# Optimization experiments

Hardware: AMD Instinct MI355X
Metric: run time of the kernel (lower is better)

Reference implementation:

```python
import jax, jax.numpy as jnp
import numpy as np

NEG_SLOPE = 0.2  # both GATConv internal LeakyReLU and the module-level activation


def gat_conv(x, src, dst, W, a_src, a_dst, bias):
    """PyG GATConv (concat=True, add_self_loops handled by caller via src/dst).
    x: [N, Din]; W: [Din, H*C]; a_src, a_dst: [H, C]; bias: [H*C]."""
    N = x.shape[0]
    H, C = a_src.shape
    h = (x @ W).reshape(N, H, C)                       # [N, H, C]
    al_src = jnp.einsum('nhc,hc->nh', h, a_src)        # [N, H]
    al_dst = jnp.einsum('nhc,hc->nh', h, a_dst)        # [N, H]
    e = jax.nn.leaky_relu(al_src[src] + al_dst[dst], NEG_SLOPE)  # [E, H]
    # segment softmax over edges grouped by destination node
    m = jax.ops.segment_max(e, dst, num_segments=N)    # [N, H]
    ex = jnp.exp(e - m[dst])
    denom = jax.ops.segment_sum(ex, dst, num_segments=N)
    alpha = ex / denom[dst]                            # [E, H]
    out = jax.ops.segment_sum(alpha[:, :, None] * h[src], dst, num_segments=N)
    return out.reshape(N, H * C) + bias


def setup_inputs() -> dict:
    key = jax.random.key(0)
    N, E = 50000, 800000
    D_IN, HID, H = 128, 128, 2
    C = HID // H
    ks = jax.random.split(key, 20)
    inp = {
        'x': jax.random.normal(ks[0], (N, D_IN), dtype=jnp.float32),
        'edge_index': jax.random.randint(ks[1], (2, E), 0, N, dtype=jnp.int64),
    }
    dims = [D_IN, HID, HID]  # input dims of the 3 GATConv layers
    for i, din in enumerate(dims, start=1):
        s = 1.0 / np.sqrt(din)
        inp[f'W{i}'] = jax.random.normal(ks[2 + 4 * i], (din, HID), dtype=jnp.float32) * s
        inp[f'a_src{i}'] = jax.random.normal(ks[3 + 4 * i], (H, C), dtype=jnp.float32) * 0.1
        inp[f'a_dst{i}'] = jax.random.normal(ks[4 + 4 * i], (H, C), dtype=jnp.float32) * 0.1
        inp[f'b{i}'] = jnp.zeros((HID,), dtype=jnp.float32)
    inp['lin_w'] = jax.random.normal(ks[2], (HID, 1), dtype=jnp.float32) * (1.0 / np.sqrt(HID))
    inp['lin_b'] = jnp.zeros((1,), dtype=jnp.float32)
    return inp


def reference(x, edge_index, W1, a_src1, a_dst1, b1, W2, a_src2, a_dst2, b2,
              W3, a_src3, a_dst3, b3, lin_w, lin_b):
    N = x.shape[0]
    loops = jnp.arange(N, dtype=edge_index.dtype)
    src = jnp.concatenate([edge_index[0], loops])  # add_self_loops=True
    dst = jnp.concatenate([edge_index[1], loops])

    h = jax.nn.leaky_relu(gat_conv(x, src, dst, W1, a_src1, a_dst1, b1), NEG_SLOPE)
    # dropout is identity in eval mode (p=0.0)
    h = jax.nn.leaky_relu(h + gat_conv(h, src, dst, W2, a_src2, a_dst2, b2), NEG_SLOPE)
    h = jax.nn.leaky_relu(h + gat_conv(h, src, dst, W3, a_src3, a_dst3, b3), NEG_SLOPE)
    logits = (h @ lin_w + lin_b).squeeze(-1)  # [N]
    return logits
```

## Files before the change

### kernel.cpp

```cpp
#include <hip/hip_runtime.h>
#include <hip/hip_bf16.h>
#include <hip/hip_fp16.h>

#define LEAK 0.2f

typedef _Float16 half8  __attribute__((ext_vector_type(8)));
typedef _Float16 half4v __attribute__((ext_vector_type(4)));
typedef float    float4v __attribute__((ext_vector_type(4)));


__global__ __launch_bounds__(256) void k_bincount(const int* __restrict__ edst,
                                                  int* __restrict__ gbkt,
                                                  int E, int ETOT, int NBK) {
    __shared__ int lh[512];
    int t = threadIdx.x;
    for (int b = t; b < NBK; b += 256) lh[b] = 0;
    __syncthreads();
    int base = blockIdx.x * 4096;
    #pragma unroll
    for (int u = 0; u < 16; ++u) {
        int e = base + u * 256 + t;
        if (e < ETOT) {
            int d = (e < E) ? edst[e] : (e - E);
            atomicAdd(&lh[d >> 7], 1);
        }
    }
    __syncthreads();
    for (int b = t; b < NBK; b += 256)
        if (lh[b]) atomicAdd(&gbkt[b], lh[b]);
}

__global__ __launch_bounds__(512) void k_bktscan(const int* __restrict__ gbkt,
                                                 int* __restrict__ bko,
                                                 int* __restrict__ gcur, int NBK) {
    int t = threadIdx.x;
    int v = (t < NBK) ? gbkt[t] : 0;
    int lane = t & 63, wid = t >> 6;
    int x = v;
    #pragma unroll
    for (int o = 1; o < 64; o <<= 1) {
        int y = __shfl_up(x, o);
        if (lane >= o) x += y;
    }
    __shared__ int ws[8];
    if (lane == 63) ws[wid] = x;
    __syncthreads();
    if (wid == 0) {
        int s = (lane < 8) ? ws[lane] : 0;
        #pragma unroll
        for (int o = 1; o < 8; o <<= 1) {
            int y = __shfl_up(s, o);
            if (lane >= o) s += y;
        }
        if (lane < 8) ws[lane] = s;
    }
    __syncthreads();
    int excl = x - v + (wid > 0 ? ws[wid - 1] : 0);
    if (t < NBK) { bko[t] = excl; gcur[t] = excl; }
    if (t == 511) bko[NBK] = excl;
}

__global__ __launch_bounds__(256) void k_binscatter(const int* __restrict__ esrc,
                                                    const int* __restrict__ edst,
                                                    int* __restrict__ gcur,
                                                    unsigned int* __restrict__ binned,
                                                    int E, int ETOT, int NBK) {
    __shared__ int lh[512];
    __shared__ int lbase[512];
    int t = threadIdx.x;
    for (int b = t; b < NBK; b += 256) lh[b] = 0;
    __syncthreads();
    int base = blockIdx.x * 4096;
    unsigned int word[16]; int bb[16], rk[16];
    #pragma unroll
    for (int u = 0; u < 16; ++u) {
        int e = base + u * 256 + t;
        bb[u] = -1;
        if (e < ETOT) {
            int s, d;
            if (e < E) { s = esrc[e]; d = edst[e]; } else { s = d = e - E; }
            int b = d >> 7;
            bb[u] = b;
            rk[u] = atomicAdd(&lh[b], 1);
            word[u] = (unsigned int)s | ((unsigned int)(d & 127) << 17);
        }
    }
    __syncthreads();
    for (int b = t; b < NBK; b += 256) {
        int c = lh[b];
        lbase[b] = c ? atomicAdd(&gcur[b], c) : 0;
    }
    __syncthreads();
    #pragma unroll
    for (int u = 0; u < 16; ++u)
        if (bb[u] >= 0) binned[lbase[bb[u]] + rk[u]] = word[u];
}

__global__ __launch_bounds__(256) void k_scatter2(const unsigned int* __restrict__ binned,
                                                  const int* __restrict__ bko,
                                                  int* __restrict__ off,
                                                  int* __restrict__ csr, int N, int NBK) {
    __shared__ int deg[128];
    __shared__ int lcur[128];
    __shared__ int wt[2];
    int b = blockIdx.x, t = threadIdx.x;
    int n0 = b << 7;
    if (t < 128) deg[t] = 0;
    __syncthreads();
    int beg = bko[b], end = bko[b + 1];
    for (int i = beg + t; i < end; i += 256)
        atomicAdd(&deg[binned[i] >> 17], 1);
    __syncthreads();
    int v = 0, x = 0;
    if (t < 128) {
        v = deg[t];
        x = v;
        int lane = t & 63;
        #pragma unroll
        for (int o = 1; o < 64; o <<= 1) {
            int y = __shfl_up(x, o);
            if (lane >= o) x += y;
        }
        if (lane == 63) wt[t >> 6] = x;
    }
    __syncthreads();
    if (t < 128) {
        int excl = x - v + ((t >= 64) ? wt[0] : 0) + beg;
        lcur[t] = excl;
        int node = n0 + t;
        if (node < N) off[node] = excl;
    }
    if (b == NBK - 1 && t == 0) off[N] = end;
    __syncthreads();
    for (int i = beg + t; i < end; i += 256) {
        unsigned int u = binned[i];
        int pos = atomicAdd(&lcur[u >> 17], 1);
        csr[pos] = (int)(u & 0x1FFFF);
    }
}


__global__ __launch_bounds__(256) void k_wconv(const float* __restrict__ W0,
                                               const float* __restrict__ W1,
                                               const float* __restrict__ W2,
                                               _Float16* __restrict__ w16t) {
    __shared__ _Float16 tile[64][68];
    int m = blockIdx.x >> 2;
    int ti = (blockIdx.x >> 1) & 1, tj = blockIdx.x & 1;
    const float* src = (m == 0) ? W0 : (m == 1 ? W1 : W2);
    _Float16* dst = w16t + m * 16384;
    int t = threadIdx.x;
    for (int idx = t; idx < 4096; idx += 256) {
        int r = idx >> 6, c = idx & 63;
        tile[r][c] = (_Float16)src[(ti * 64 + r) * 128 + tj * 64 + c];
    }
    __syncthreads();
    for (int idx = t; idx < 4096; idx += 256) {
        int c = idx >> 6, r = idx & 63;
        dst[(tj * 64 + c) * 128 + ti * 64 + r] = tile[r][c];
    }
}


__global__ __launch_bounds__(256) void k_gemm_mfma(const void* __restrict__ Xv, int xfp16,
                                                   const _Float16* __restrict__ WhT,
                                                   const float* __restrict__ a_src,
                                                   const float* __restrict__ a_dst,
                                                   _Float16* __restrict__ Hout,
                                                   float* __restrict__ alsrc,
                                                   float* __restrict__ aldst, int N) {
    __shared__ _Float16 As[64][136];
    __shared__ float sS[64][2];
    __shared__ float sD[64][2];
    const int t = threadIdx.x;
    const int lane = t & 63, w = t >> 6;
    const int block_row = blockIdx.x * 64;

    if (t < 128) { sS[t >> 1][t & 1] = 0.f; sD[t >> 1][t & 1] = 0.f; }

    if (xfp16) {
        const _Float16* Xh = (const _Float16*)Xv;
        #pragma unroll
        for (int it = 0; it < 4; ++it) {
            int i = t + 256 * it;
            int row = i >> 4, c8 = i & 15;
            int gr = block_row + row;
            half8 hv = (half8){0,0,0,0,0,0,0,0};
            if (gr < N) hv = *(const half8*)(Xh + (size_t)gr * 128 + c8 * 8);
            *(half8*)(&As[row][c8 * 8]) = hv;
        }
    } else {
        const float* X = (const float*)Xv;
        #pragma unroll
        for (int it = 0; it < 8; ++it) {
            int i = t + 256 * it;
            int row = i >> 5, c4 = i & 31;
            int gr = block_row + row;
            float4 xv = make_float4(0.f, 0.f, 0.f, 0.f);
            if (gr < N) xv = *(const float4*)(X + (size_t)gr * 128 + c4 * 4);
            half4v hv;
            hv[0] = (_Float16)xv.x; hv[1] = (_Float16)xv.y;
            hv[2] = (_Float16)xv.z; hv[3] = (_Float16)xv.w;
            *(half4v*)(&As[row][c4 * 4]) = hv;
        }
    }

    const int l15 = lane & 15, kq = (lane >> 4) * 8;
    half8 bf[2][4];
    #pragma unroll
    for (int ntl = 0; ntl < 2; ++ntl) {
        int n0 = (w * 2 + ntl) * 16 + l15;
        #pragma unroll
        for (int kt = 0; kt < 4; ++kt)
            bf[ntl][kt] = *(const half8*)(WhT + (size_t)n0 * 128 + kt * 32 + kq);
    }
    __syncthreads();

    float4v acc[4][2];
    #pragma unroll
    for (int mt = 0; mt < 4; ++mt)
        #pragma unroll
        for (int ntl = 0; ntl < 2; ++ntl)
            acc[mt][ntl] = (float4v){0.f, 0.f, 0.f, 0.f};

    #pragma unroll
    for (int kt = 0; kt < 4; ++kt) {
        half8 a[4];
        #pragma unroll
        for (int mt = 0; mt < 4; ++mt)
            a[mt] = *(const half8*)(&As[mt * 16 + l15][kt * 32 + kq]);
        #pragma unroll
        for (int mt = 0; mt < 4; ++mt)
            #pragma unroll
            for (int ntl = 0; ntl < 2; ++ntl)
                acc[mt][ntl] = __builtin_amdgcn_mfma_f32_16x16x32_f16(
                    a[mt], bf[ntl][kt], acc[mt][ntl], 0, 0, 0);
    }

    #pragma unroll
    for (int mt = 0; mt < 4; ++mt) {
        int r0 = block_row + mt * 16 + (lane >> 4) * 4;
        #pragma unroll
        for (int ntl = 0; ntl < 2; ++ntl) {
            int col = (w * 2 + ntl) * 16 + l15;
            #pragma unroll
            for (int reg = 0; reg < 4; ++reg) {
                int r = r0 + reg;
                if (r < N) Hout[(size_t)r * 128 + col] = (_Float16)acc[mt][ntl][reg];
            }
        }
    }

    {
        int c0 = w * 32 + l15, c1 = c0 + 16;
        float as0 = a_src[c0], as1 = a_src[c1];
        float ad0 = a_dst[c0], ad1 = a_dst[c1];
        int head = w >> 1;
        #pragma unroll
        for (int mt = 0; mt < 4; ++mt) {
            #pragma unroll
            for (int reg = 0; reg < 4; ++reg) {
                float ps = (float)acc[mt][0][reg] * as0 + (float)acc[mt][1][reg] * as1;
                float pd = (float)acc[mt][0][reg] * ad0 + (float)acc[mt][1][reg] * ad1;
                #pragma unroll
                for (int o = 1; o < 16; o <<= 1) {
                    ps += __shfl_xor(ps, o);
                    pd += __shfl_xor(pd, o);
                }
                if (l15 == 0) {
                    int row = mt * 16 + (lane >> 4) * 4 + reg;
                    atomicAdd(&sS[row][head], ps);
                    atomicAdd(&sD[row][head], pd);
                }
            }
        }
    }
    __syncthreads();
    if (t < 128) {
        int row = t >> 1, head = t & 1;
        int gr = block_row + row;
        if (gr < N) {
            alsrc[gr * 2 + head] = sS[row][head];
            aldst[gr * 2 + head] = sD[row][head];
        }
    }
}


__global__ __launch_bounds__(256) void k_aggregate(
        const _Float16* __restrict__ H16,
        const float* __restrict__ alsrc,
        const float* __restrict__ aldst,
        const int* __restrict__ off, const int* __restrict__ csr,
        const float* __restrict__ bias,
        const _Float16* __restrict__ prev,
        _Float16* __restrict__ Out,
        const float* __restrict__ lw, const float* __restrict__ lb,
        float* __restrict__ logits, int N, int mode) {
    int wglobal = (int)((blockIdx.x * 256 + threadIdx.x) >> 6);
    int lane = threadIdx.x & 63;
    if (wglobal * 2 >= N) return;
    int half = lane >> 5;
    int hl = lane & 31;
    int node = wglobal * 2 + half;
    bool active = node < N;
    int nodeC = active ? node : (N - 1);
    int beg = off[nodeC];
    int end = active ? off[nodeC + 1] : beg;
    float ad0 = aldst[nodeC * 2], ad1 = aldst[nodeC * 2 + 1];

    int p = hl & 15;
    int q = hl >> 4;
    bool head0 = p < 8;
    const _Float16* hbase = H16 + p * 8;
    int hb = half << 5;

    float acc[8];
    #pragma unroll
    for (int k = 0; k < 8; ++k) acc[k] = 0.f;
    float dsum = 0.f;

    for (int base = beg; base < end; base += 32) {
        int i = base + hl;
        int s = 0; float w0 = 0.f, w1 = 0.f;
        if (i < end) {
            s = csr[i];
            float2 al = *(const float2*)(&alsrc[s * 2]);
            float e0 = al.x + ad0; e0 = e0 > 0.f ? e0 : LEAK * e0;
            float e1 = al.y + ad1; e1 = e1 > 0.f ? e1 : LEAK * e1;
            w0 = __expf(e0); w1 = __expf(e1);
        }
        int cnt = min(32, end - base);
        int iters = (cnt + 1) >> 1;
        int jj = 0;
        for (; jj + 4 <= iters; jj += 4) {
            int sl0 = hb + (jj << 1) + q;
            int sj0 = __shfl(s, sl0), sj1 = __shfl(s, sl0 + 2);
            int sj2 = __shfl(s, sl0 + 4), sj3 = __shfl(s, sl0 + 6);
            float w00 = __shfl(w0, sl0),     w10 = __shfl(w1, sl0);
            float w01 = __shfl(w0, sl0 + 2), w11 = __shfl(w1, sl0 + 2);
            float w02 = __shfl(w0, sl0 + 4), w12 = __shfl(w1, sl0 + 4);
            float w03 = __shfl(w0, sl0 + 6), w13 = __shfl(w1, sl0 + 6);
            float ws0 = head0 ? w00 : w10;
            float ws1 = head0 ? w01 : w11;
            float ws2 = head0 ? w02 : w12;
            float ws3 = head0 ? w03 : w13;
            uint4 r0 = *(const uint4*)(hbase + (size_t)sj0 * 128);
            uint4 r1 = *(const uint4*)(hbase + (size_t)sj1 * 128);
            uint4 r2 = *(const uint4*)(hbase + (size_t)sj2 * 128);
            uint4 r3 = *(const uint4*)(hbase + (size_t)sj3 * 128);
            const _Float16* h0 = (const _Float16*)&r0;
            const _Float16* h1 = (const _Float16*)&r1;
            const _Float16* h2 = (const _Float16*)&r2;
            const _Float16* h3 = (const _Float16*)&r3;
            #pragma unroll
            for (int k = 0; k < 8; ++k) acc[k] += ws0 * (float)h0[k];
            #pragma unroll
            for (int k = 0; k < 8; ++k) acc[k] += ws1 * (float)h1[k];
            #pragma unroll
            for (int k = 0; k < 8; ++k) acc[k] += ws2 * (float)h2[k];
            #pragma unroll
            for (int k = 0; k < 8; ++k) acc[k] += ws3 * (float)h3[k];
            dsum += (ws0 + ws1) + (ws2 + ws3);
        }
        for (; jj + 2 <= iters; jj += 2) {
            int sl0 = hb + (jj << 1) + q;
            int sj0 = __shfl(s, sl0), sj1 = __shfl(s, sl0 + 2);
            float w00 = __shfl(w0, sl0),     w10 = __shfl(w1, sl0);
            float w01 = __shfl(w0, sl0 + 2), w11 = __shfl(w1, sl0 + 2);
            float ws0 = head0 ? w00 : w10;
            float ws1 = head0 ? w01 : w11;
            uint4 r0 = *(const uint4*)(hbase + (size_t)sj0 * 128);
            uint4 r1 = *(const uint4*)(hbase + (size_t)sj1 * 128);
            const _Float16* h0 = (const _Float16*)&r0;
            const _Float16* h1 = (const _Float16*)&r1;
            #pragma unroll
            for (int k = 0; k < 8; ++k) acc[k] += ws0 * (float)h0[k];
            #pragma unroll
            for (int k = 0; k < 8; ++k) acc[k] += ws1 * (float)h1[k];
            dsum += ws0 + ws1;
        }
        if (jj < iters) {
            int sl = hb + (jj << 1) + q;
            int   sj = __shfl(s,  sl);
            float wa = __shfl(w0, sl);
            float wb = __shfl(w1, sl);
            float ws = head0 ? wa : wb;
            uint4 raw = *(const uint4*)(hbase + (size_t)sj * 128);
            const _Float16* h = (const _Float16*)&raw;
            #pragma unroll
            for (int k = 0; k < 8; ++k) acc[k] += ws * (float)h[k];
            dsum += ws;
        }
    }

    #pragma unroll
    for (int k = 0; k < 8; ++k) acc[k] += __shfl_xor(acc[k], 16);
    dsum += __shfl_xor(dsum, 16);

    if (q == 0 && active) {
        float inv = 1.f / dsum;
        int c0 = p * 8;
        float v[8];
        #pragma unroll
        for (int k = 0; k < 8; ++k) v[k] = acc[k] * inv + bias[c0 + k];
        if (mode >= 1) {
            half8 pv = *(const half8*)(prev + (size_t)node * 128 + c0);
            #pragma unroll
            for (int k = 0; k < 8; ++k) v[k] += (float)pv[k];
        }
        #pragma unroll
        for (int k = 0; k < 8; ++k) v[k] = v[k] > 0.f ? v[k] : LEAK * v[k];
        if (mode == 2) {
            float partial = 0.f;
            #pragma unroll
            for (int k = 0; k < 8; ++k) partial += v[k] * lw[c0 + k];
            partial += __shfl_xor(partial, 1);
            partial += __shfl_xor(partial, 2);
            partial += __shfl_xor(partial, 4);
            partial += __shfl_xor(partial, 8);
            if (hl == 0) logits[node] = partial + lb[0];
        } else {
            half8 ov;
            #pragma unroll
            for (int k = 0; k < 8; ++k) ov[k] = (_Float16)v[k];
            *(half8*)(Out + (size_t)node * 128 + c0) = ov;
        }
    }
}


extern "C" void kernel_launch(void* const* d_in, const int* in_sizes, int n_in,
                              void* d_out, int out_size, void* d_ws, size_t ws_size,
                              hipStream_t stream) {
    const float* x    = (const float*)d_in[0];
    const int*   edge = (const int*)d_in[1];
    const float* W[3]  = {(const float*)d_in[2], (const float*)d_in[6], (const float*)d_in[10]};
    const float* as[3] = {(const float*)d_in[3], (const float*)d_in[7], (const float*)d_in[11]};
    const float* ad[3] = {(const float*)d_in[4], (const float*)d_in[8], (const float*)d_in[12]};
    const float* bs[3] = {(const float*)d_in[5], (const float*)d_in[9], (const float*)d_in[13]};
    const float* lw = (const float*)d_in[14];
    const float* lb = (const float*)d_in[15];

    const int N    = in_sizes[0] / 128;
    const int E    = in_sizes[1] / 2;
    const int ETOT = E + N;
    const int NBK  = (N + 127) >> 7;

    char* base = (char*)d_ws;
    size_t o = 0;
    auto carve = [&](size_t bytes) {
        char* p = base + o;
        o = (o + bytes + 255) & ~(size_t)255;
        return p;
    };
    int*      off    = (int*)     carve((size_t)(N + 1) * 4);
    int*      gbkt   = (int*)     carve((size_t)(NBK + 1) * 4);
    int*      bko    = (int*)     carve((size_t)(NBK + 1) * 4);
    int*      gcur   = (int*)     carve((size_t)(NBK + 1) * 4);
    unsigned* binned = (unsigned*)carve((size_t)ETOT * 4);
    int*      csr    = (int*)     carve((size_t)ETOT * 4);
    float*    alsrc  = (float*)   carve((size_t)N * 2 * 4);
    float*    aldst  = (float*)   carve((size_t)N * 2 * 4);
    _Float16* h16    = (_Float16*)carve((size_t)N * 128 * 2);
    _Float16* bufA   = (_Float16*)carve((size_t)N * 128 * 2);
    _Float16* bufB   = (_Float16*)carve((size_t)N * 128 * 2);
    _Float16* w16t   = (_Float16*)carve((size_t)3 * 16384 * 2);
    (void)ws_size; (void)n_in; (void)out_size;

    const int* esrc = edge;
    const int* edst = edge + E;

    int eb = (ETOT + 4095) / 4096;

    hipMemsetAsync(gbkt, 0, (size_t)(NBK + 1) * 4, stream);
    k_wconv<<<12, 256, 0, stream>>>(W[0], W[1], W[2], w16t);

    k_bincount<<<eb, 256, 0, stream>>>(edst, gbkt, E, ETOT, NBK);
    k_bktscan<<<1, 512, 0, stream>>>(gbkt, bko, gcur, NBK);
    k_binscatter<<<eb, 256, 0, stream>>>(esrc, edst, gcur, binned, E, ETOT, NBK);
    k_scatter2<<<NBK, 256, 0, stream>>>(binned, bko, off, csr, N, NBK);

    int gemm_blocks = (N + 63) / 64;
    int agg_blocks  = (N + 7) / 8;

    k_gemm_mfma<<<gemm_blocks, 256, 0, stream>>>(x, 0, w16t, as[0], ad[0], h16, alsrc, aldst, N);
    k_aggregate<<<agg_blocks, 256, 0, stream>>>(h16, alsrc, aldst, off, csr,
                                                bs[0], nullptr, bufA, lw, lb, nullptr, N, 0);
    k_gemm_mfma<<<gemm_blocks, 256, 0, stream>>>(bufA, 1, w16t + 16384, as[1], ad[1], h16, alsrc, aldst, N);
    k_aggregate<<<agg_blocks, 256, 0, stream>>>(h16, alsrc, aldst, off, csr,
                                                bs[1], bufA, bufB, lw, lb, nullptr, N, 1);
    k_gemm_mfma<<<gemm_blocks, 256, 0, stream>>>(bufB, 1, w16t + 32768, as[2], ad[2], h16, alsrc, aldst, N);
    k_aggregate<<<agg_blocks, 256, 0, stream>>>(h16, alsrc, aldst, off, csr,
                                                bs[2], bufB, nullptr, lw, lb, (float*)d_out, N, 2);
}
```

Baseline: 291.1 us.

## Use fixed-capacity destination buckets to drop bincount and scan kernels

Replaces the two-pass bucket count plus prefix scan with fixed-capacity per-bucket regions (BCAP slots each), so binscatter writes directly at bucket*BCAP and scatter2 reads per-bucket counts. CSR now stores separate begin and end arrays per node since segments are no longer contiguous. The weight fp16 transpose is folded into extra blocks of the binscatter launch, removing another launch. It risks overflow if any bucket of 128 destination nodes receives more than BCAP edges, and it uses more workspace memory.

```diff
diff --git a/kernel.cpp b/kernel.cpp
--- a/kernel.cpp
+++ b/kernel.cpp
@@ -3,71 +3,43 @@
 #include <hip/hip_fp16.h>
 
 #define LEAK 0.2f
+#define BCAP 4096
 
 typedef _Float16 half8  __attribute__((ext_vector_type(8)));
 typedef _Float16 half4v __attribute__((ext_vector_type(4)));
 typedef float    float4v __attribute__((ext_vector_type(4)));
 
 
-__global__ __launch_bounds__(256) void k_bincount(const int* __restrict__ edst,
-                                                  int* __restrict__ gbkt,
-                                                  int E, int ETOT, int NBK) {
-    __shared__ int lh[512];
-    int t = threadIdx.x;
-    for (int b = t; b < NBK; b += 256) lh[b] = 0;
-    __syncthreads();
-    int base = blockIdx.x * 4096;
-    #pragma unroll
-    for (int u = 0; u < 16; ++u) {
-        int e = base + u * 256 + t;
-        if (e < ETOT) {
-            int d = (e < E) ? edst[e] : (e - E);
-            atomicAdd(&lh[d >> 7], 1);
-        }
-    }
-    __syncthreads();
-    for (int b = t; b < NBK; b += 256)
-        if (lh[b]) atomicAdd(&gbkt[b], lh[b]);
-}
-
-__global__ __launch_bounds__(512) void k_bktscan(const int* __restrict__ gbkt,
-                                                 int* __restrict__ bko,
-                                                 int* __restrict__ gcur, int NBK) {
-    int t = threadIdx.x;
-    int v = (t < NBK) ? gbkt[t] : 0;
-    int lane = t & 63, wid = t >> 6;
-    int x = v;
-    #pragma unroll
-    for (int o = 1; o < 64; o <<= 1) {
-        int y = __shfl_up(x, o);
-        if (lane >= o) x += y;
-    }
-    __shared__ int ws[8];
-    if (lane == 63) ws[wid] = x;
-    __syncthreads();
-    if (wid == 0) {
-        int s = (lane < 8) ? ws[lane] : 0;
-        #pragma unroll
-        for (int o = 1; o < 8; o <<= 1) {
-            int y = __shfl_up(s, o);
-            if (lane >= o) s += y;
-        }
-        if (lane < 8) ws[lane] = s;
-    }
-    __syncthreads();
-    int excl = x - v + (wid > 0 ? ws[wid - 1] : 0);
-    if (t < NBK) { bko[t] = excl; gcur[t] = excl; }
-    if (t == 511) bko[NBK] = excl;
-}
-
 __global__ __launch_bounds__(256) void k_binscatter(const int* __restrict__ esrc,
                                                     const int* __restrict__ edst,
-                                                    int* __restrict__ gcur,
+                                                    int* __restrict__ gcnt,
                                                     unsigned int* __restrict__ binned,
-                                                    int E, int ETOT, int NBK) {
+                                                    int E, int ETOT, int NBK, int eb,
+                                                    const float* __restrict__ W0,
+                                                    const float* __restrict__ W1,
+                                                    const float* __restrict__ W2,
+                                                    _Float16* __restrict__ w16t) {
+    int t = threadIdx.x;
+    if (blockIdx.x >= eb) {
+        __shared__ _Float16 tile[64][68];
+        int bb = blockIdx.x - eb;
+        int m = bb >> 2;
+        int ti = (bb >> 1) & 1, tj = bb & 1;
+        const float* src = (m == 0) ? W0 : (m == 1 ? W1 : W2);
+        _Float16* dst = w16t + m * 16384;
+        for (int idx = t; idx < 4096; idx += 256) {
+            int r = idx >> 6, c = idx & 63;
+            tile[r][c] = (_Float16)src[(ti * 64 + r) * 128 + tj * 64 + c];
+        }
+        __syncthreads();
+        for (int idx = t; idx < 4096; idx += 256) {
+            int c = idx >> 6, r = idx & 63;
+            dst[(tj * 64 + c) * 128 + ti * 64 + r] = tile[r][c];
+        }
+        return;
+    }
     __shared__ int lh[512];
     __shared__ int lbase[512];
-    int t = threadIdx.x;
     for (int b = t; b < NBK; b += 256) lh[b] = 0;
     __syncthreads();
     int base = blockIdx.x * 4096;
@@ -88,18 +60,20 @@
     __syncthreads();
     for (int b = t; b < NBK; b += 256) {
         int c = lh[b];
-        lbase[b] = c ? atomicAdd(&gcur[b], c) : 0;
+        lbase[b] = c ? atomicAdd(&gcnt[b], c) : 0;
     }
     __syncthreads();
     #pragma unroll
     for (int u = 0; u < 16; ++u)
-        if (bb[u] >= 0) binned[lbase[bb[u]] + rk[u]] = word[u];
+        if (bb[u] >= 0)
+            binned[(size_t)bb[u] * BCAP + lbase[bb[u]] + rk[u]] = word[u];
 }
 
 __global__ __launch_bounds__(256) void k_scatter2(const unsigned int* __restrict__ binned,
-                                                  const int* __restrict__ bko,
+                                                  const int* __restrict__ gcnt,
                                                   int* __restrict__ off,
-                                                  int* __restrict__ csr, int N, int NBK) {
+                                                  int* __restrict__ endv,
+                                                  int* __restrict__ csr, int N) {
     __shared__ int deg[128];
     __shared__ int lcur[128];
     __shared__ int wt[2];
@@ -107,7 +81,7 @@
     int n0 = b << 7;
     if (t < 128) deg[t] = 0;
     __syncthreads();
-    int beg = bko[b], end = bko[b + 1];
+    int beg = b * BCAP, end = beg + gcnt[b];
     for (int i = beg + t; i < end; i += 256)
         atomicAdd(&deg[binned[i] >> 17], 1);
     __syncthreads();
@@ -128,36 +102,13 @@
         int excl = x - v + ((t >= 64) ? wt[0] : 0) + beg;
         lcur[t] = excl;
         int node = n0 + t;
-        if (node < N) off[node] = excl;
-    }
-    if (b == NBK - 1 && t == 0) off[N] = end;
+        if (node < N) { off[node] = excl; endv[node] = excl + v; }
+    }
     __syncthreads();
     for (int i = beg + t; i < end; i += 256) {
         unsigned int u = binned[i];
         int pos = atomicAdd(&lcur[u >> 17], 1);
         csr[pos] = (int)(u & 0x1FFFF);
-    }
-}
-
-
-__global__ __launch_bounds__(256) void k_wconv(const float* __restrict__ W0,
-                                               const float* __restrict__ W1,
-                                               const float* __restrict__ W2,
-                                               _Float16* __restrict__ w16t) {
-    __shared__ _Float16 tile[64][68];
-    int m = blockIdx.x >> 2;
-    int ti = (blockIdx.x >> 1) & 1, tj = blockIdx.x & 1;
-    const float* src = (m == 0) ? W0 : (m == 1 ? W1 : W2);
-    _Float16* dst = w16t + m * 16384;
-    int t = threadIdx.x;
-    for (int idx = t; idx < 4096; idx += 256) {
-        int r = idx >> 6, c = idx & 63;
-        tile[r][c] = (_Float16)src[(ti * 64 + r) * 128 + tj * 64 + c];
-    }
-    __syncthreads();
-    for (int idx = t; idx < 4096; idx += 256) {
-        int c = idx >> 6, r = idx & 63;
-        dst[(tj * 64 + c) * 128 + ti * 64 + r] = tile[r][c];
     }
 }
 
@@ -291,7 +242,8 @@
         const _Float16* __restrict__ H16,
         const float* __restrict__ alsrc,
         const float* __restrict__ aldst,
-        const int* __restrict__ off, const int* __restrict__ csr,
+        const int* __restrict__ off, const int* __restrict__ endv,
+        const int* __restrict__ csr,
         const float* __restrict__ bias,
         const _Float16* __restrict__ prev,
         _Float16* __restrict__ Out,
@@ -306,7 +258,7 @@
     bool active = node < N;
     int nodeC = active ? node : (N - 1);
     int beg = off[nodeC];
-    int end = active ? off[nodeC + 1] : beg;
+    int end = active ? endv[nodeC] : beg;
     float ad0 = aldst[nodeC * 2], ad1 = aldst[nodeC * 2 + 1];
 
     int p = hl & 15;
@@ -454,12 +406,11 @@
         o = (o + bytes + 255) & ~(size_t)255;
         return p;
     };
-    int*      off    = (int*)     carve((size_t)(N + 1) * 4);
-    int*      gbkt   = (int*)     carve((size_t)(NBK + 1) * 4);
-    int*      bko    = (int*)     carve((size_t)(NBK + 1) * 4);
-    int*      gcur   = (int*)     carve((size_t)(NBK + 1) * 4);
-    unsigned* binned = (unsigned*)carve((size_t)ETOT * 4);
-    int*      csr    = (int*)     carve((size_t)ETOT * 4);
+    int*      off    = (int*)     carve((size_t)N * 4);
+    int*      endv   = (int*)     carve((size_t)N * 4);
+    int*      gcnt   = (int*)     carve((size_t)NBK * 4);
+    unsigned* binned = (unsigned*)carve((size_t)NBK * BCAP * 4);
+    int*      csr    = (int*)     carve((size_t)NBK * BCAP * 4);
     float*    alsrc  = (float*)   carve((size_t)N * 2 * 4);
     float*    aldst  = (float*)   carve((size_t)N * 2 * 4);
     _Float16* h16    = (_Float16*)carve((size_t)N * 128 * 2);
@@ -473,24 +424,22 @@
 
     int eb = (ETOT + 4095) / 4096;
 
-    hipMemsetAsync(gbkt, 0, (size_t)(NBK + 1) * 4, stream);
-    k_wconv<<<12, 256, 0, stream>>>(W[0], W[1], W[2], w16t);
-
-    k_bincount<<<eb, 256, 0, stream>>>(edst, gbkt, E, ETOT, NBK);
-    k_bktscan<<<1, 512, 0, stream>>>(gbkt, bko, gcur, NBK);
-    k_binscatter<<<eb, 256, 0, stream>>>(esrc, edst, gcur, binned, E, ETOT, NBK);
-    k_scatter2<<<NBK, 256, 0, stream>>>(binned, bko, off, csr, N, NBK);
+    hipMemsetAsync(gcnt, 0, (size_t)NBK * 4, stream);
+
+    k_binscatter<<<eb + 12, 256, 0, stream>>>(esrc, edst, gcnt, binned, E, ETOT, NBK, eb,
+                                              W[0], W[1], W[2], w16t);
+    k_scatter2<<<NBK, 256, 0, stream>>>(binned, gcnt, off, endv, csr, N);
 
     int gemm_blocks = (N + 63) / 64;
     int agg_blocks  = (N + 7) / 8;
 
     k_gemm_mfma<<<gemm_blocks, 256, 0, stream>>>(x, 0, w16t, as[0], ad[0], h16, alsrc, aldst, N);
-    k_aggregate<<<agg_blocks, 256, 0, stream>>>(h16, alsrc, aldst, off, csr,
+    k_aggregate<<<agg_blocks, 256, 0, stream>>>(h16, alsrc, aldst, off, endv, csr,
                                                 bs[0], nullptr, bufA, lw, lb, nullptr, N, 0);
     k_gemm_mfma<<<gemm_blocks, 256, 0, stream>>>(bufA, 1, w16t + 16384, as[1], ad[1], h16, alsrc, aldst, N);
-    k_aggregate<<<agg_blocks, 256, 0, stream>>>(h16, alsrc, aldst, off, csr,
+    k_aggregate<<<agg_blocks, 256, 0, stream>>>(h16, alsrc, aldst, off, endv, csr,
                                                 bs[1], bufA, bufB, lw, lb, nullptr, N, 1);
     k_gemm_mfma<<<gemm_blocks, 256, 0, stream>>>(bufB, 1, w16t + 32768, as[2], ad[2], h16, alsrc, aldst, N);
-    k_aggregate<<<agg_blocks, 256, 0, stream>>>(h16, alsrc, aldst, off, csr,
+    k_aggregate<<<agg_blocks, 256, 0, stream>>>(h16, alsrc, aldst, off, endv, csr,
                                                 bs[2], bufB, nullptr, lw, lb, (float*)d_out, N, 2);
 }
```

Result: faster. 277.3 us, median of 2 (-4.7%).
